# Kernel tuning notes

Hardware: AMD Instinct MI355X
Metric: run time of the kernel (lower is better)

## Reference

```python
import jax, jax.numpy as jnp
import numpy as np

OUT_H = OUT_W = 15      # POOLER_RESOLUTION (template / pooler_z path)
SCALE = 0.0625          # POOLER_SCALES: 1/16 feature stride
SR = 2                  # POOLER_SAMPLING_RATIO
IMG = 1024.0


def setup_inputs() -> dict:
    key = jax.random.key(0)
    k1, k2, k3, k4, k5 = jax.random.split(key, 5)
    x = jax.random.normal(k1, (2, 256, 64, 64), dtype=jnp.float32)
    N = 512
    cx = jax.random.uniform(k2, (N,), minval=32.0, maxval=IMG - 32.0)
    cy = jax.random.uniform(k3, (N,), minval=32.0, maxval=IMG - 32.0)
    wh = jax.random.uniform(k4, (N, 2), minval=32.0, maxval=160.0)
    x1 = jnp.clip(cx - wh[:, 0] / 2, 0.0, IMG - 1)
    x2 = jnp.clip(cx + wh[:, 0] / 2, 0.0, IMG - 1)
    y1 = jnp.clip(cy - wh[:, 1] / 2, 0.0, IMG - 1)
    y2 = jnp.clip(cy + wh[:, 1] / 2, 0.0, IMG - 1)
    boxes = jnp.stack([x1, y1, x2, y2], axis=1).astype(jnp.float32)
    batch_idx = jax.random.randint(k5, (N,), 0, 2, dtype=jnp.int32)
    return {"x": x, "boxes": boxes, "batch_idx": batch_idx}


def _axis_idx(p, size):
    """ROIAlign bilinear index/frac/validity along one axis. p: [N, K] float."""
    valid = (p >= -1.0) & (p <= size)
    p = jnp.clip(p, 0.0, size - 1.0)
    lo = jnp.floor(p).astype(jnp.int32)
    lo = jnp.minimum(lo, size - 1)
    hi = jnp.minimum(lo + 1, size - 1)
    frac = p - lo.astype(p.dtype)  # 0 when lo==size-1 (matches torch clamp)
    return lo, hi, frac, valid


def roi_align(feats, boxes, batch_idx, out_h, out_w, scale, sr):
    B, C, H, W = feats.shape
    b = boxes * scale
    x1, y1, x2, y2 = b[:, 0], b[:, 1], b[:, 2], b[:, 3]
    roi_w = jnp.maximum(x2 - x1, 1.0)
    roi_h = jnp.maximum(y2 - y1, 1.0)
    bin_w = roi_w / out_w
    bin_h = roi_h / out_h
    # sample point k along an axis: start + (k + 0.5)/sr * bin  (k = ph*sr + iy)
    ky = (jnp.arange(out_h * sr, dtype=feats.dtype) + 0.5) / sr
    kx = (jnp.arange(out_w * sr, dtype=feats.dtype) + 0.5) / sr
    ys = y1[:, None] + ky[None, :] * bin_h[:, None]  # [N, out_h*sr]
    xs = x1[:, None] + kx[None, :] * bin_w[:, None]  # [N, out_w*sr]
    ylo, yhi, fy, vy = _axis_idx(ys, H)
    xlo, xhi, fx, vx = _axis_idx(xs, W)
    bi = batch_idx[:, None, None]

    def gather(yi, xi):
        # feats[b, :, y, x] -> [N, out_h*sr, out_w*sr, C]
        return feats[bi, :, yi[:, :, None], xi[:, None, :]]

    wy_lo = (1.0 - fy) * vy
    wy_hi = fy * vy
    wx_lo = (1.0 - fx) * vx
    wx_hi = fx * vx

    def w2(wy, wx):
        return (wy[:, :, None] * wx[:, None, :])[..., None]  # [N,Hs,Ws,1]

    val = (w2(wy_lo, wx_lo) * gather(ylo, xlo)
           + w2(wy_lo, wx_hi) * gather(ylo, xhi)
           + w2(wy_hi, wx_lo) * gather(yhi, xlo)
           + w2(wy_hi, wx_hi) * gather(yhi, xhi))
    N = boxes.shape[0]
    val = val.reshape(N, out_h, sr, out_w, sr, C).mean(axis=(2, 4))
    return jnp.transpose(val, (0, 3, 1, 2))  # [N, C, out_h, out_w]


def reference(x, boxes, batch_idx):
    # EMMFeatureExtractor.forward with sr=None -> pooler_z (template ROIAlign 15x15)
    return roi_align(x, boxes, batch_idx, OUT_H, OUT_W, SCALE, SR)
```

## Files before the change

### kernel.cpp

```cpp
#include <hip/hip_runtime.h>

constexpr int NROI = 512;
constexpr int CCH  = 256;
constexpr int HH   = 64;
constexpr int WWd  = 64;
constexpr int OHh  = 15;
constexpr int OWw  = 15;
constexpr float SCL = 0.0625f;
constexpr int TSTR  = 17;
constexpr int TROWS = 16;
constexpr int CHUNK  = 64;
constexpr int NCHUNK = CCH / CHUNK;

__global__ __launch_bounds__(256, 4)
void roi_align_kernel(const float* __restrict__ x,
                      const float* __restrict__ boxes,
                      const int* __restrict__ bidx,
                      float* __restrict__ out) {
  __shared__ float T[4][TROWS * TSTR];
  __shared__ float wx_s[OWw][3];
  __shared__ float wy_s[OHh][3];
  __shared__ int   jb_s[OWw];
  __shared__ int   rb_s[OHh];

  const int roi = blockIdx.x >> 2;
  const int g   = blockIdx.x & 3;
  const int t   = threadIdx.x;

  if (t < 32) {
    const int axis = t >> 4;
    const int o    = t & 15;
    if (o < OHh) {
      const float p1v = boxes[roi * 4 + axis] * SCL;
      const float p2v = boxes[roi * 4 + 2 + axis] * SCL;
      const float sz  = fmaxf(p2v - p1v, 1.0f);
      const float bin = sz * (1.0f / 15.0f);
      int lo[2]; float wl[2], wh[2];
#pragma unroll
      for (int s = 0; s < 2; ++s) {
        float p = p1v + ((float)(2 * o + s) + 0.5f) * 0.5f * bin;
        const float valid = (p >= -1.0f && p <= 64.0f) ? 0.5f : 0.0f;
        p = fminf(fmaxf(p, 0.0f), 63.0f);
        const int l = (int)p;
        const float f = p - (float)l;
        lo[s] = l; wl[s] = (1.0f - f) * valid; wh[s] = f * valid;
      }
      const int base = min(lo[0], WWd - 3);
      float w[3] = {0.f, 0.f, 0.f};
#pragma unroll
      for (int s = 0; s < 2; ++s) {
        const int hi = min(lo[s] + 1, WWd - 1);
        w[lo[s] - base] += wl[s];
        w[hi - base]    += wh[s];
      }
      if (axis == 0) { jb_s[o] = base; wx_s[o][0] = w[0]; wx_s[o][1] = w[1]; wx_s[o][2] = w[2]; }
      else           { rb_s[o] = base; wy_s[o][0] = w[0]; wy_s[o][1] = w[1]; wy_s[o][2] = w[2]; }
    }
  }
  __syncthreads();

  const int r0 = rb_s[0];
  const int R  = rb_s[OHh - 1] + 3 - r0;
  const int bi = bidx[roi];

  const bool hasA = (t < R * OWw);
  float ax0 = 0.f, ax1 = 0.f, ax2 = 0.f;
  const float* aptr = x;
  int aT = 0;
  if (hasA) {
    const int ar = t / OWw, aw = t - ar * OWw;
    ax0 = wx_s[aw][0]; ax1 = wx_s[aw][1]; ax2 = wx_s[aw][2];
    aptr = x + (((size_t)bi * CCH + g * CHUNK) * HH + (size_t)(r0 + ar)) * WWd + jb_s[aw];
    aT = ar * TSTR + aw;
  }

  const bool hasB = (t < OHh * OWw);
  float by0 = 0.f, by1 = 0.f, by2 = 0.f;
  int bT = 0;
  float* optr = out;
  if (hasB) {
    const int oh = t / OWw;
    by0 = wy_s[oh][0]; by1 = wy_s[oh][1]; by2 = wy_s[oh][2];
    bT = (rb_s[oh] - r0) * TSTR + (t - oh * OWw);
    optr = out + ((size_t)roi * CCH + (size_t)g * CHUNK) * (OHh * OWw) + t;
  }

  constexpr size_t CSTR = (size_t)HH * WWd;
  constexpr int OSTR = OHh * OWw;

  for (int it = 0; it < CHUNK / 2; ++it) {
    float* T0 = T[(it & 1) * 2];
    float* T1 = T[(it & 1) * 2 + 1];
    if (hasA) {
      const float* p0 = aptr;
      const float* p1 = aptr + CSTR;
      const float v0 = fmaf(p0[0], ax0, fmaf(p0[1], ax1, p0[2] * ax2));
      const float v1 = fmaf(p1[0], ax0, fmaf(p1[1], ax1, p1[2] * ax2));
      T0[aT] = v0;
      T1[aT] = v1;
      aptr += 2 * CSTR;
    }
    __syncthreads();
    if (hasB) {
      const float a0 = T0[bT], a1 = T0[bT + TSTR], a2 = T0[bT + 2 * TSTR];
      const float b0 = T1[bT], b1 = T1[bT + TSTR], b2 = T1[bT + 2 * TSTR];
      const float o0 = fmaf(a0, by0, fmaf(a1, by1, a2 * by2));
      const float o1 = fmaf(b0, by0, fmaf(b1, by1, b2 * by2));
      __builtin_nontemporal_store(o0, optr);
      __builtin_nontemporal_store(o1, optr + OSTR);
      optr += 2 * OSTR;
    }
  }
}

extern "C" void kernel_launch(void* const* d_in, const int* in_sizes, int n_in,
                              void* d_out, int out_size, void* d_ws, size_t ws_size,
                              hipStream_t stream) {
  const float* x     = (const float*)d_in[0];
  const float* boxes = (const float*)d_in[1];
  const int*   bid   = (const int*)d_in[2];
  float* out = (float*)d_out;
  hipLaunchKernelGGL(roi_align_kernel, dim3(NROI * NCHUNK), dim3(256), 0, stream,
                     x, boxes, bid, out);
}
```

Baseline: 156.3 us.

## Remap threads to (channel, output column) and drop per-channel block barriers

Work is reassigned so each thread owns one output column of one channel (16 channels per pass, 4 passes per block). The horizontally interpolated rows now sit in a private slice of shared memory, and the per-channel __syncthreads and double buffering are gone. The vertical weights and packed row offsets are held in registers. This removes block-wide barriers and idle threads, but makes global loads strided across channels instead of coalesced along rows, and adds register pressure from the 45 vertical weights.

```diff
diff --git a/kernel.cpp b/kernel.cpp
--- a/kernel.cpp
+++ b/kernel.cpp
@@ -8,16 +8,15 @@
 constexpr int OWw  = 15;
 constexpr float SCL = 0.0625f;
 constexpr int TSTR  = 17;
-constexpr int TROWS = 16;
-constexpr int CHUNK  = 64;
-constexpr int NCHUNK = CCH / CHUNK;
+constexpr int CPB   = 64;
+constexpr int KIT   = CPB / 16;
 
 __global__ __launch_bounds__(256, 4)
 void roi_align_kernel(const float* __restrict__ x,
                       const float* __restrict__ boxes,
                       const int* __restrict__ bidx,
                       float* __restrict__ out) {
-  __shared__ float T[4][TROWS * TSTR];
+  __shared__ float T[256 * TSTR];
   __shared__ float wx_s[OWw][3];
   __shared__ float wy_s[OHh][3];
   __shared__ int   jb_s[OWw];
@@ -63,52 +62,50 @@
   const int R  = rb_s[OHh - 1] + 3 - r0;
   const int bi = bidx[roi];
 
-  const bool hasA = (t < R * OWw);
+  const int ow = t & 15;
+  const int cs = t >> 4;
+  const bool act = (ow < OWw);
+
+  float wy[OHh][3];
+#pragma unroll
+  for (int oh = 0; oh < OHh; ++oh) {
+    wy[oh][0] = wy_s[oh][0]; wy[oh][1] = wy_s[oh][1]; wy[oh][2] = wy_s[oh][2];
+  }
+  unsigned rp0 = 0, rp1 = 0;
+#pragma unroll
+  for (int oh = 0; oh < 8; ++oh)  rp0 |= (unsigned)(rb_s[oh] - r0) << (4 * oh);
+#pragma unroll
+  for (int oh = 8; oh < OHh; ++oh) rp1 |= (unsigned)(rb_s[oh] - r0) << (4 * (oh - 8));
+
   float ax0 = 0.f, ax1 = 0.f, ax2 = 0.f;
-  const float* aptr = x;
-  int aT = 0;
-  if (hasA) {
-    const int ar = t / OWw, aw = t - ar * OWw;
-    ax0 = wx_s[aw][0]; ax1 = wx_s[aw][1]; ax2 = wx_s[aw][2];
-    aptr = x + (((size_t)bi * CCH + g * CHUNK) * HH + (size_t)(r0 + ar)) * WWd + jb_s[aw];
-    aT = ar * TSTR + aw;
-  }
+  int jb = 0;
+  if (act) { ax0 = wx_s[ow][0]; ax1 = wx_s[ow][1]; ax2 = wx_s[ow][2]; jb = jb_s[ow]; }
 
-  const bool hasB = (t < OHh * OWw);
-  float by0 = 0.f, by1 = 0.f, by2 = 0.f;
-  int bT = 0;
-  float* optr = out;
-  if (hasB) {
-    const int oh = t / OWw;
-    by0 = wy_s[oh][0]; by1 = wy_s[oh][1]; by2 = wy_s[oh][2];
-    bT = (rb_s[oh] - r0) * TSTR + (t - oh * OWw);
-    optr = out + ((size_t)roi * CCH + (size_t)g * CHUNK) * (OHh * OWw) + t;
-  }
-
-  constexpr size_t CSTR = (size_t)HH * WWd;
+  float* Tp = &T[t * TSTR];
+  const int NR2 = (R + 1) >> 1;
   constexpr int OSTR = OHh * OWw;
 
-  for (int it = 0; it < CHUNK / 2; ++it) {
-    float* T0 = T[(it & 1) * 2];
-    float* T1 = T[(it & 1) * 2 + 1];
-    if (hasA) {
-      const float* p0 = aptr;
-      const float* p1 = aptr + CSTR;
-      const float v0 = fmaf(p0[0], ax0, fmaf(p0[1], ax1, p0[2] * ax2));
-      const float v1 = fmaf(p1[0], ax0, fmaf(p1[1], ax1, p1[2] * ax2));
-      T0[aT] = v0;
-      T1[aT] = v1;
-      aptr += 2 * CSTR;
-    }
-    __syncthreads();
-    if (hasB) {
-      const float a0 = T0[bT], a1 = T0[bT + TSTR], a2 = T0[bT + 2 * TSTR];
-      const float b0 = T1[bT], b1 = T1[bT + TSTR], b2 = T1[bT + 2 * TSTR];
-      const float o0 = fmaf(a0, by0, fmaf(a1, by1, a2 * by2));
-      const float o1 = fmaf(b0, by0, fmaf(b1, by1, b2 * by2));
-      __builtin_nontemporal_store(o0, optr);
-      __builtin_nontemporal_store(o1, optr + OSTR);
-      optr += 2 * OSTR;
+  for (int k = 0; k < KIT; ++k) {
+    const int ch = g * CPB + k * 16 + cs;
+    const float* fbase = x + ((size_t)(bi * CCH + ch) * HH) * WWd + jb;
+    if (act) {
+      for (int it = 0; it < NR2; ++it) {
+        const int ra  = r0 + 2 * it;
+        const int rb2 = min(ra + 1, HH - 1);
+        const float* pa = fbase + ra * WWd;
+        const float* pb = fbase + rb2 * WWd;
+        Tp[2 * it]     = fmaf(pa[0], ax0, fmaf(pa[1], ax1, pa[2] * ax2));
+        Tp[2 * it + 1] = fmaf(pb[0], ax0, fmaf(pb[1], ax1, pb[2] * ax2));
+      }
+      float* obase = out + ((size_t)roi * CCH + ch) * OSTR + ow;
+#pragma unroll
+      for (int oh = 0; oh < OHh; ++oh) {
+        const unsigned rr = (oh < 8) ? ((rp0 >> (4 * oh)) & 15u)
+                                     : ((rp1 >> (4 * (oh - 8))) & 15u);
+        const float* q = Tp + rr;
+        const float v = fmaf(q[0], wy[oh][0], fmaf(q[1], wy[oh][1], q[2] * wy[oh][2]));
+        __builtin_nontemporal_store(v, obase + oh * OWw);
+      }
     }
   }
 }
@@ -120,6 +117,6 @@
   const float* boxes = (const float*)d_in[1];
   const int*   bid   = (const int*)d_in[2];
   float* out = (float*)d_out;
-  hipLaunchKernelGGL(roi_align_kernel, dim3(NROI * NCHUNK), dim3(256), 0, stream,
+  hipLaunchKernelGGL(roi_align_kernel, dim3(NROI * 4), dim3(256), 0, stream,
                      x, boxes, bid, out);
 }
```

New measurement: 173.3 us. 10.9% more time.
